# Optimization experiments

Hardware: AMD Instinct MI355X
Metric: run time of the kernel (lower is better)

The kernel has to match this reference:

```python
import jax, jax.numpy as jnp
import numpy as np

B, N, F, K = 512, 128, 128, 4


def setup_inputs() -> dict:
    key = jax.random.key(0)
    ks = jax.random.split(key, 12)
    # xavier-normal-ish scales
    s_rw = float(np.sqrt(2.0 / (F + F)))
    s_sw = float(np.sqrt(2.0 / (F + F)))
    inp = {
        "H": jax.random.normal(ks[0], (B, N, F), dtype=jnp.float32),
        "E": jax.random.uniform(ks[1], (B, N, N, K), dtype=jnp.float32),
        "RW1": jax.random.normal(ks[2], (F, F, K), dtype=jnp.float32) * s_rw,
        "SW1": jax.random.normal(ks[3], (F, F), dtype=jnp.float32) * s_sw,
        "RW2": jax.random.normal(ks[4], (F, F, K), dtype=jnp.float32) * s_rw,
        "SW2": jax.random.normal(ks[5], (F, F), dtype=jnp.float32) * s_sw,
        "RW3": jax.random.normal(ks[6], (F, F, K), dtype=jnp.float32) * s_rw,
        "SW3": jax.random.normal(ks[7], (F, F), dtype=jnp.float32) * s_sw,
        "W1": jax.random.normal(ks[8], (F, 20), dtype=jnp.float32) * float(np.sqrt(1.0 / F)),
        "b1": jnp.zeros((20,), dtype=jnp.float32),
        "W2": jax.random.normal(ks[9], (20, 1), dtype=jnp.float32) * float(np.sqrt(1.0 / 20)),
        "b2": jnp.zeros((1,), dtype=jnp.float32),
    }
    return inp


def _rgcn_conv(H, E, D, RW, SW):
    # einsum('bi,bijk,bjm,mnk->bin') done in two GEMM-shaped steps
    M = jnp.einsum('bijk,bjm->bimk', E, H)          # [B,N,F,K]
    msg = jnp.einsum('bimk,mnk->bin', M, RW)        # [B,N,F]
    return jax.nn.sigmoid(msg * D[:, :, None] + jnp.einsum('bij,jl->bil', H, SW))


def reference(H, E, RW1, SW1, RW2, SW2, RW3, SW3, W1, b1, W2, b2):
    # degree norm with self-loops: (E + eye)[b,i,:,:].sum() = E.sum((2,3)) + K
    k = jnp.asarray(E.shape[-1], dtype=E.dtype)
    D = 1.0 / (E.sum(axis=(2, 3)) + k)              # [B,N]
    H = _rgcn_conv(H, E, D, RW1, SW1)
    H = _rgcn_conv(H, E, D, RW2, SW2)
    H = _rgcn_conv(H, E, D, RW3, SW3)
    h = jnp.maximum(H @ W1 + b1, 0.1 * (H @ W1 + b1))  # LeakyReLU(0.1)
    score = jnp.mean(jax.nn.sigmoid(h @ W2 + b2))
    return score
```

## Files before the change

### kernel.cpp

```cpp
#include <hip/hip_runtime.h>
#include <math.h>

#define BB 512
#define NN 128
#define FF 128
#define KK 4

typedef __attribute__((ext_vector_type(8))) short bf16x8;
typedef __attribute__((ext_vector_type(4))) float f32x4;

__device__ inline unsigned short f2bf(float x) {
  union { float f; unsigned int u; } v; v.f = x;
  unsigned int r = v.u + 0x7fff + ((v.u >> 16) & 1);
  return (unsigned short)(r >> 16);
}
__device__ inline float bf2f(unsigned short h) {
  union { unsigned int u; float f; } v; v.u = ((unsigned int)h) << 16; return v.f;
}

__device__ inline void g2l16(const unsigned short* gptr, unsigned short* lptr) {
  __builtin_amdgcn_global_load_lds(
      (const __attribute__((address_space(1))) unsigned int*)gptr,
      (__attribute__((address_space(3))) unsigned int*)lptr, 16, 0, 0);
}

__global__ __launch_bounds__(256) void k_convE(const float* __restrict__ E,
                                               unsigned short* __restrict__ Eb,
                                               float* __restrict__ Dv) {
  int wave = threadIdx.x >> 6;
  int lane = threadIdx.x & 63;
  int row  = blockIdx.x * 4 + wave;
  const float* p = E + (size_t)row * 512 + lane * 8;
  f32x4 a = *(const f32x4*)p;
  f32x4 b = *(const f32x4*)(p + 4);
  float s = a[0] + a[1] + a[2] + a[3] + b[0] + b[1] + b[2] + b[3];
  #pragma unroll
  for (int off = 32; off > 0; off >>= 1) s += __shfl_down(s, off, 64);
  if (lane == 0) Dv[row] = 1.0f / (s + 4.0f);
  union { unsigned short h[8]; f32x4 v; } u;
  u.h[0] = f2bf(a[0]); u.h[1] = f2bf(a[1]); u.h[2] = f2bf(a[2]); u.h[3] = f2bf(a[3]);
  u.h[4] = f2bf(b[0]); u.h[5] = f2bf(b[1]); u.h[6] = f2bf(b[2]); u.h[7] = f2bf(b[3]);
  *(f32x4*)(Eb + (size_t)row * 512 + lane * 8) = u.v;
}

__global__ __launch_bounds__(256) void k_convH(const float* __restrict__ H,
                                               unsigned short* __restrict__ Hb) {
  size_t i = ((size_t)blockIdx.x * 256 + threadIdx.x) * 8;
  f32x4 a = *(const f32x4*)(H + i);
  f32x4 b = *(const f32x4*)(H + i + 4);
  union { unsigned short h[8]; f32x4 v; } u;
  u.h[0] = f2bf(a[0]); u.h[1] = f2bf(a[1]); u.h[2] = f2bf(a[2]); u.h[3] = f2bf(a[3]);
  u.h[4] = f2bf(b[0]); u.h[5] = f2bf(b[1]); u.h[6] = f2bf(b[2]); u.h[7] = f2bf(b[3]);
  *(f32x4*)(Hb + i) = u.v;
}

__global__ __launch_bounds__(256) void k_buildW(const float* __restrict__ RW,
                                                const float* __restrict__ SW,
                                                unsigned short* __restrict__ W2) {
  int idx = blockIdx.x * 256 + threadIdx.x;
  int m = idx & 127;
  int c = idx >> 7;
  float v = (c < 512) ? RW[m * 512 + c] : SW[m * 128 + (c - 512)];
  W2[idx] = f2bf(v);
}

#define GS_PITCH 132

__global__ __launch_bounds__(512, 2) void k_layer(
    const unsigned short* __restrict__ Eb,
    const unsigned short* __restrict__ Hin,
    const unsigned short* __restrict__ W2L,
    const float* __restrict__ Dv,
    unsigned short* __restrict__ Hout)
{
  __shared__ unsigned short Gs[128 * GS_PITCH];
  __shared__ unsigned short Es[128 * 128];

  const int b = blockIdx.x;
  const unsigned short* E_b = Eb  + (size_t)b * 65536;
  const unsigned short* H_b = Hin + (size_t)b * 16384;

  const int tid = threadIdx.x;
  const int w = tid >> 6, l = tid & 63;
  const int wr = w >> 1, wc = w & 1;
  const int lq = l >> 4, lm = l & 15;

  f32x4 macc[2][4] = {};

  for (int s = 0; s < 4; ++s) {
    if (s) __syncthreads();

    bf16x8 fa0[4], fb0[2];
    #pragma unroll
    for (int f = 0; f < 4; ++f)
      fa0[f] = *(const bf16x8*)(W2L + (w * 64 + f * 16 + lm) * 128 + lq * 8);
    #pragma unroll
    for (int g = 0; g < 2; ++g)
      fb0[g] = *(const bf16x8*)(H_b + (s * 32 + g * 16 + lm) * 128 + lq * 8);

    #pragma unroll
    for (int r = 0; r < 4; ++r) {
      int R   = r * 32 + w * 4 + (l >> 4);
      int cbg = (l & 15) ^ (R & 15);
      g2l16(E_b + R * 512 + s * 128 + cbg * 8,
            Es + (r * 32 + w * 4) * 128);
    }

    f32x4 gacc[4][2] = {};
    #pragma unroll
    for (int f = 0; f < 4; ++f)
      #pragma unroll
      for (int g = 0; g < 2; ++g)
        gacc[f][g] = __builtin_amdgcn_mfma_f32_16x16x32_bf16(fa0[f], fb0[g], gacc[f][g], 0, 0, 0);
    #pragma unroll
    for (int k0 = 32; k0 < 128; k0 += 32) {
      bf16x8 fa[4], fb[2];
      #pragma unroll
      for (int f = 0; f < 4; ++f)
        fa[f] = *(const bf16x8*)(W2L + (w * 64 + f * 16 + lm) * 128 + k0 + lq * 8);
      #pragma unroll
      for (int g = 0; g < 2; ++g)
        fb[g] = *(const bf16x8*)(H_b + (s * 32 + g * 16 + lm) * 128 + k0 + lq * 8);
      #pragma unroll
      for (int f = 0; f < 4; ++f)
        #pragma unroll
        for (int g = 0; g < 2; ++g)
          gacc[f][g] = __builtin_amdgcn_mfma_f32_16x16x32_bf16(fa[f], fb[g], gacc[f][g], 0, 0, 0);
    }
    #pragma unroll
    for (int f = 0; f < 4; ++f) {
      int n = w * 16 + f * 4 + lq;
      #pragma unroll
      for (int g = 0; g < 2; ++g) {
        int jl = g * 16 + lm;
        union { unsigned short h4[4]; uint2 v; } u;
        u.h4[0] = f2bf(gacc[f][g][0]); u.h4[1] = f2bf(gacc[f][g][1]);
        u.h4[2] = f2bf(gacc[f][g][2]); u.h4[3] = f2bf(gacc[f][g][3]);
        *(uint2*)(&Gs[n * GS_PITCH + jl * 4]) = u.v;
      }
    }
    __syncthreads();

    #pragma unroll
    for (int kt = 0; kt < 4; ++kt) {
      bf16x8 ea[2], fb[4];
      #pragma unroll
      for (int f = 0; f < 2; ++f) {
        int i  = wr * 32 + f * 16 + lm;
        int cb = (kt * 4 + lq) ^ lm;
        ea[f] = *(const bf16x8*)(Es + i * 128 + cb * 8);
      }
      #pragma unroll
      for (int g = 0; g < 4; ++g)
        fb[g] = *(const bf16x8*)(&Gs[(wc * 64 + g * 16 + lm) * GS_PITCH + kt * 32 + lq * 8]);
      #pragma unroll
      for (int f = 0; f < 2; ++f)
        #pragma unroll
        for (int g = 0; g < 4; ++g)
          macc[f][g] = __builtin_amdgcn_mfma_f32_16x16x32_bf16(ea[f], fb[g], macc[f][g], 0, 0, 0);
    }
  }

  f32x4 sacc[2][4] = {};
  #pragma unroll
  for (int k0 = 0; k0 < 128; k0 += 32) {
    bf16x8 fa[2], fb[4];
    #pragma unroll
    for (int f = 0; f < 2; ++f)
      fa[f] = *(const bf16x8*)(H_b + (wr * 32 + f * 16 + lm) * 128 + k0 + lq * 8);
    #pragma unroll
    for (int g = 0; g < 4; ++g)
      fb[g] = *(const bf16x8*)(W2L + (512 + wc * 64 + g * 16 + lm) * 128 + k0 + lq * 8);
    #pragma unroll
    for (int f = 0; f < 2; ++f)
      #pragma unroll
      for (int g = 0; g < 4; ++g)
        sacc[f][g] = __builtin_amdgcn_mfma_f32_16x16x32_bf16(fa[f], fb[g], sacc[f][g], 0, 0, 0);
  }

  const float* dvb = Dv + b * 128;
  __syncthreads();
  #pragma unroll
  for (int f = 0; f < 2; ++f) {
    int i0 = wr * 32 + f * 16 + lq * 4;
    f32x4 d = *(const f32x4*)(dvb + i0);
    #pragma unroll
    for (int g = 0; g < 4; ++g) {
      int n = wc * 64 + g * 16 + lm;
      #pragma unroll
      for (int r = 0; r < 4; ++r) {
        float v = fmaf(macc[f][g][r], d[r], sacc[f][g][r]);
        Es[(i0 + r) * 128 + n] = f2bf(1.0f / (1.0f + __expf(-v)));
      }
    }
  }
  __syncthreads();
  unsigned short* O_b = Hout + (size_t)b * 16384;
  {
    int off = tid * 32;
    f32x4 v0 = *(const f32x4*)(Es + off);
    f32x4 v1 = *(const f32x4*)(Es + off + 8);
    f32x4 v2 = *(const f32x4*)(Es + off + 16);
    f32x4 v3 = *(const f32x4*)(Es + off + 24);
    *(f32x4*)(O_b + off)      = v0;
    *(f32x4*)(O_b + off + 8)  = v1;
    *(f32x4*)(O_b + off + 16) = v2;
    *(f32x4*)(O_b + off + 24) = v3;
  }
}

__global__ __launch_bounds__(256) void k_mlp(
    const unsigned short* __restrict__ H,
    const float* __restrict__ W1,
    const float* __restrict__ b1,
    const float* __restrict__ W2,
    const float* __restrict__ b2,
    float* __restrict__ sumOut)
{
  __shared__ float W1s[128 * 20];
  __shared__ float b1s[20], W2s[20];
  __shared__ float red[256];
  for (int i = threadIdx.x; i < 2560; i += 256) W1s[i] = W1[i];
  if (threadIdx.x < 20) { b1s[threadIdx.x] = b1[threadIdx.x]; W2s[threadIdx.x] = W2[threadIdx.x]; }
  __syncthreads();

  int row = blockIdx.x * 256 + threadIdx.x;
  float h[20];
  #pragma unroll
  for (int j = 0; j < 20; ++j) h[j] = b1s[j];
  const unsigned short* hr = H + (size_t)row * 128;
  for (int m8 = 0; m8 < 128; m8 += 8) {
    f32x4 pk = *(const f32x4*)(hr + m8);
    const unsigned short* us = (const unsigned short*)&pk;
    #pragma unroll
    for (int e = 0; e < 8; ++e) {
      float x = bf2f(us[e]);
      #pragma unroll
      for (int j = 0; j < 20; ++j) h[j] = fmaf(x, W1s[(m8 + e) * 20 + j], h[j]);
    }
  }
  float v = b2[0];
  #pragma unroll
  for (int j = 0; j < 20; ++j) {
    float t = h[j];
    t = fmaxf(t, 0.1f * t);
    v = fmaf(t, W2s[j], v);
  }
  float s = 1.0f / (1.0f + __expf(-v));

  red[threadIdx.x] = s;
  __syncthreads();
  #pragma unroll
  for (int off = 128; off > 0; off >>= 1) {
    if (threadIdx.x < off) red[threadIdx.x] += red[threadIdx.x + off];
    __syncthreads();
  }
  if (threadIdx.x == 0) atomicAdd(sumOut, red[0]);
}

__global__ void k_final(const float* __restrict__ sum, float* __restrict__ out) {
  out[0] = sum[0] * (1.0f / 65536.0f);
}

extern "C" void kernel_launch(void* const* d_in, const int* in_sizes, int n_in,
                              void* d_out, int out_size, void* d_ws, size_t ws_size,
                              hipStream_t stream) {
  const float* H   = (const float*)d_in[0];
  const float* E   = (const float*)d_in[1];
  const float* RW1 = (const float*)d_in[2];
  const float* SW1 = (const float*)d_in[3];
  const float* RW2 = (const float*)d_in[4];
  const float* SW2 = (const float*)d_in[5];
  const float* RW3 = (const float*)d_in[6];
  const float* SW3 = (const float*)d_in[7];
  const float* W1  = (const float*)d_in[8];
  const float* b1  = (const float*)d_in[9];
  const float* W2  = (const float*)d_in[10];
  const float* b2  = (const float*)d_in[11];
  float* out = (float*)d_out;

  char* w = (char*)d_ws;
  float*          wsD   = (float*)w;           w += (size_t)65536 * 4;
  unsigned short* wsEb  = (unsigned short*)w;  w += (size_t)33554432 * 2;
  unsigned short* wsHa  = (unsigned short*)w;  w += (size_t)8388608 * 2;
  unsigned short* wsHb  = (unsigned short*)w;  w += (size_t)8388608 * 2;
  unsigned short* wsW2  = (unsigned short*)w;  w += (size_t)3 * 81920 * 2;
  float*          wsSum = (float*)w;           w += 256;

  k_convE<<<BB * NN / 4, 256, 0, stream>>>(E, wsEb, wsD);
  k_convH<<<8388608 / (256 * 8), 256, 0, stream>>>(H, wsHa);
  k_buildW<<<320, 256, 0, stream>>>(RW1, SW1, wsW2);
  k_buildW<<<320, 256, 0, stream>>>(RW2, SW2, wsW2 + 81920);
  k_buildW<<<320, 256, 0, stream>>>(RW3, SW3, wsW2 + 163840);
  hipMemsetAsync(wsSum, 0, sizeof(float), stream);

  k_layer<<<BB, 512, 0, stream>>>(wsEb, wsHa, wsW2,          wsD, wsHb);
  k_layer<<<BB, 512, 0, stream>>>(wsEb, wsHb, wsW2 + 81920,  wsD, wsHa);
  k_layer<<<BB, 512, 0, stream>>>(wsEb, wsHa, wsW2 + 163840, wsD, wsHb);

  k_mlp<<<BB * NN / 256, 256, 0, stream>>>(wsHb, W1, b1, W2, b2, wsSum);
  k_final<<<1, 1, 0, stream>>>(wsSum, out);
}
```

Before: 432.9 us.

## Fuse prep kernels and all three layers plus MLP into one megakernel

Merges the E/H conversion and weight-building kernels into a single prep launch. It also fuses the three RGCN layers, the MLP and the final reduction into one per-graph kernel that finishes with an atomic counter, removing launch gaps and the memset. Each graph's layers run back to back in the same block, so its E slice may stay hot in cache across layers. The cost is extra intermediate H buffers, a last-block-done pattern that relies on threadfence ordering, and MLP work that uses only 128 of the 512 threads.

```diff
diff --git a/kernel.cpp b/kernel.cpp
--- a/kernel.cpp
+++ b/kernel.cpp
@@ -5,6 +5,7 @@
 #define NN 128
 #define FF 128
 #define KK 4
+#define GS_PITCH 132
 
 typedef __attribute__((ext_vector_type(8))) short bf16x8;
 typedef __attribute__((ext_vector_type(4))) float f32x4;
@@ -24,63 +25,61 @@
       (__attribute__((address_space(3))) unsigned int*)lptr, 16, 0, 0);
 }
 
-__global__ __launch_bounds__(256) void k_convE(const float* __restrict__ E,
-                                               unsigned short* __restrict__ Eb,
-                                               float* __restrict__ Dv) {
-  int wave = threadIdx.x >> 6;
-  int lane = threadIdx.x & 63;
-  int row  = blockIdx.x * 4 + wave;
-  const float* p = E + (size_t)row * 512 + lane * 8;
-  f32x4 a = *(const f32x4*)p;
-  f32x4 b = *(const f32x4*)(p + 4);
-  float s = a[0] + a[1] + a[2] + a[3] + b[0] + b[1] + b[2] + b[3];
-  #pragma unroll
-  for (int off = 32; off > 0; off >>= 1) s += __shfl_down(s, off, 64);
-  if (lane == 0) Dv[row] = 1.0f / (s + 4.0f);
-  union { unsigned short h[8]; f32x4 v; } u;
-  u.h[0] = f2bf(a[0]); u.h[1] = f2bf(a[1]); u.h[2] = f2bf(a[2]); u.h[3] = f2bf(a[3]);
-  u.h[4] = f2bf(b[0]); u.h[5] = f2bf(b[1]); u.h[6] = f2bf(b[2]); u.h[7] = f2bf(b[3]);
-  *(f32x4*)(Eb + (size_t)row * 512 + lane * 8) = u.v;
-}
-
-__global__ __launch_bounds__(256) void k_convH(const float* __restrict__ H,
-                                               unsigned short* __restrict__ Hb) {
-  size_t i = ((size_t)blockIdx.x * 256 + threadIdx.x) * 8;
-  f32x4 a = *(const f32x4*)(H + i);
-  f32x4 b = *(const f32x4*)(H + i + 4);
-  union { unsigned short h[8]; f32x4 v; } u;
-  u.h[0] = f2bf(a[0]); u.h[1] = f2bf(a[1]); u.h[2] = f2bf(a[2]); u.h[3] = f2bf(a[3]);
-  u.h[4] = f2bf(b[0]); u.h[5] = f2bf(b[1]); u.h[6] = f2bf(b[2]); u.h[7] = f2bf(b[3]);
-  *(f32x4*)(Hb + i) = u.v;
-}
-
-__global__ __launch_bounds__(256) void k_buildW(const float* __restrict__ RW,
-                                                const float* __restrict__ SW,
-                                                unsigned short* __restrict__ W2) {
-  int idx = blockIdx.x * 256 + threadIdx.x;
-  int m = idx & 127;
-  int c = idx >> 7;
-  float v = (c < 512) ? RW[m * 512 + c] : SW[m * 128 + (c - 512)];
-  W2[idx] = f2bf(v);
-}
-
-#define GS_PITCH 132
-
-__global__ __launch_bounds__(512, 2) void k_layer(
-    const unsigned short* __restrict__ Eb,
-    const unsigned short* __restrict__ Hin,
-    const unsigned short* __restrict__ W2L,
-    const float* __restrict__ Dv,
-    unsigned short* __restrict__ Hout)
+__global__ __launch_bounds__(256) void k_prep(
+    const float* __restrict__ E, const float* __restrict__ H,
+    const float* __restrict__ RW1, const float* __restrict__ SW1,
+    const float* __restrict__ RW2, const float* __restrict__ SW2,
+    const float* __restrict__ RW3, const float* __restrict__ SW3,
+    unsigned short* __restrict__ Eb, unsigned short* __restrict__ Ha,
+    unsigned short* __restrict__ W2L, float* __restrict__ Dv,
+    float* __restrict__ Sum, int* __restrict__ Cnt)
 {
-  __shared__ unsigned short Gs[128 * GS_PITCH];
-  __shared__ unsigned short Es[128 * 128];
-
-  const int b = blockIdx.x;
-  const unsigned short* E_b = Eb  + (size_t)b * 65536;
-  const unsigned short* H_b = Hin + (size_t)b * 16384;
-
-  const int tid = threadIdx.x;
+  const int bid = blockIdx.x;
+  if (bid < 16384) {
+    int wave = threadIdx.x >> 6;
+    int lane = threadIdx.x & 63;
+    int row  = bid * 4 + wave;
+    const float* p = E + (size_t)row * 512 + lane * 8;
+    f32x4 a = *(const f32x4*)p;
+    f32x4 b = *(const f32x4*)(p + 4);
+    float s = a[0] + a[1] + a[2] + a[3] + b[0] + b[1] + b[2] + b[3];
+    #pragma unroll
+    for (int off = 32; off > 0; off >>= 1) s += __shfl_down(s, off, 64);
+    if (lane == 0) Dv[row] = 1.0f / (s + 4.0f);
+    union { unsigned short h[8]; f32x4 v; } u;
+    u.h[0] = f2bf(a[0]); u.h[1] = f2bf(a[1]); u.h[2] = f2bf(a[2]); u.h[3] = f2bf(a[3]);
+    u.h[4] = f2bf(b[0]); u.h[5] = f2bf(b[1]); u.h[6] = f2bf(b[2]); u.h[7] = f2bf(b[3]);
+    *(f32x4*)(Eb + (size_t)row * 512 + lane * 8) = u.v;
+  } else if (bid < 20480) {
+    size_t i = ((size_t)(bid - 16384) * 256 + threadIdx.x) * 8;
+    f32x4 a = *(const f32x4*)(H + i);
+    f32x4 b = *(const f32x4*)(H + i + 4);
+    union { unsigned short h[8]; f32x4 v; } u;
+    u.h[0] = f2bf(a[0]); u.h[1] = f2bf(a[1]); u.h[2] = f2bf(a[2]); u.h[3] = f2bf(a[3]);
+    u.h[4] = f2bf(b[0]); u.h[5] = f2bf(b[1]); u.h[6] = f2bf(b[2]); u.h[7] = f2bf(b[3]);
+    *(f32x4*)(Ha + i) = u.v;
+  } else {
+    int t2  = bid - 20480;
+    int tab = t2 / 320;
+    int idx = (t2 - tab * 320) * 256 + threadIdx.x;
+    int m = idx & 127;
+    int c = idx >> 7;
+    const float* RW = (tab == 0) ? RW1 : (tab == 1) ? RW2 : RW3;
+    const float* SW = (tab == 0) ? SW1 : (tab == 1) ? SW2 : SW3;
+    float v = (c < 512) ? RW[m * 512 + c] : SW[m * 128 + (c - 512)];
+    W2L[(size_t)tab * 81920 + idx] = f2bf(v);
+    if (t2 == 0 && threadIdx.x == 0) { *Sum = 0.0f; *Cnt = 0; }
+  }
+}
+
+__device__ __forceinline__ void layer_body(
+    const unsigned short* __restrict__ E_b,
+    const unsigned short* __restrict__ H_b,
+    const unsigned short* __restrict__ W2c,
+    const float* __restrict__ dvb,
+    unsigned short* __restrict__ O_b,
+    unsigned short* Gs, unsigned short* Es, const int tid)
+{
   const int w = tid >> 6, l = tid & 63;
   const int wr = w >> 1, wc = w & 1;
   const int lq = l >> 4, lm = l & 15;
@@ -93,7 +92,7 @@
     bf16x8 fa0[4], fb0[2];
     #pragma unroll
     for (int f = 0; f < 4; ++f)
-      fa0[f] = *(const bf16x8*)(W2L + (w * 64 + f * 16 + lm) * 128 + lq * 8);
+      fa0[f] = *(const bf16x8*)(W2c + (w * 64 + f * 16 + lm) * 128 + lq * 8);
     #pragma unroll
     for (int g = 0; g < 2; ++g)
       fb0[g] = *(const bf16x8*)(H_b + (s * 32 + g * 16 + lm) * 128 + lq * 8);
@@ -117,7 +116,7 @@
       bf16x8 fa[4], fb[2];
       #pragma unroll
       for (int f = 0; f < 4; ++f)
-        fa[f] = *(const bf16x8*)(W2L + (w * 64 + f * 16 + lm) * 128 + k0 + lq * 8);
+        fa[f] = *(const bf16x8*)(W2c + (w * 64 + f * 16 + lm) * 128 + k0 + lq * 8);
       #pragma unroll
       for (int g = 0; g < 2; ++g)
         fb[g] = *(const bf16x8*)(H_b + (s * 32 + g * 16 + lm) * 128 + k0 + lq * 8);
@@ -170,7 +169,7 @@
       fa[f] = *(const bf16x8*)(H_b + (wr * 32 + f * 16 + lm) * 128 + k0 + lq * 8);
     #pragma unroll
     for (int g = 0; g < 4; ++g)
-      fb[g] = *(const bf16x8*)(W2L + (512 + wc * 64 + g * 16 + lm) * 128 + k0 + lq * 8);
+      fb[g] = *(const bf16x8*)(W2c + (512 + wc * 64 + g * 16 + lm) * 128 + k0 + lq * 8);
     #pragma unroll
     for (int f = 0; f < 2; ++f)
       #pragma unroll
@@ -178,7 +177,6 @@
         sacc[f][g] = __builtin_amdgcn_mfma_f32_16x16x32_bf16(fa[f], fb[g], sacc[f][g], 0, 0, 0);
   }
 
-  const float* dvb = Dv + b * 128;
   __syncthreads();
   #pragma unroll
   for (int f = 0; f < 2; ++f) {
@@ -195,7 +193,6 @@
     }
   }
   __syncthreads();
-  unsigned short* O_b = Hout + (size_t)b * 16384;
   {
     int off = tid * 32;
     f32x4 v0 = *(const f32x4*)(Es + off);
@@ -207,64 +204,90 @@
     *(f32x4*)(O_b + off + 16) = v2;
     *(f32x4*)(O_b + off + 24) = v3;
   }
-}
-
-__global__ __launch_bounds__(256) void k_mlp(
-    const unsigned short* __restrict__ H,
-    const float* __restrict__ W1,
-    const float* __restrict__ b1,
-    const float* __restrict__ W2,
-    const float* __restrict__ b2,
-    float* __restrict__ sumOut)
+  __syncthreads();
+}
+
+__global__ __launch_bounds__(512, 2) void k_mega(
+    const unsigned short* __restrict__ Eb,
+    const unsigned short* __restrict__ Ha,
+    unsigned short* __restrict__ Hb,
+    unsigned short* __restrict__ Hc,
+    unsigned short* __restrict__ Hd,
+    const unsigned short* __restrict__ W2L,
+    const float* __restrict__ Dv,
+    const float* __restrict__ W1, const float* __restrict__ b1,
+    const float* __restrict__ W2w, const float* __restrict__ b2,
+    float* __restrict__ Sum, int* __restrict__ Cnt,
+    float* __restrict__ out)
 {
-  __shared__ float W1s[128 * 20];
-  __shared__ float b1s[20], W2s[20];
-  __shared__ float red[256];
-  for (int i = threadIdx.x; i < 2560; i += 256) W1s[i] = W1[i];
-  if (threadIdx.x < 20) { b1s[threadIdx.x] = b1[threadIdx.x]; W2s[threadIdx.x] = W2[threadIdx.x]; }
-  __syncthreads();
-
-  int row = blockIdx.x * 256 + threadIdx.x;
-  float h[20];
+  __shared__ unsigned short Gs[128 * GS_PITCH];
+  __shared__ unsigned short Es[128 * 128];
+
+  const int b = blockIdx.x;
+  const int tid = threadIdx.x;
+  const unsigned short* E_b = Eb + (size_t)b * 65536;
+  const float* dvb = Dv + b * 128;
+
+  layer_body(E_b, Ha + (size_t)b * 16384, W2L,          dvb, Hb + (size_t)b * 16384, Gs, Es, tid);
+  layer_body(E_b, Hb + (size_t)b * 16384, W2L + 81920,  dvb, Hc + (size_t)b * 16384, Gs, Es, tid);
+  layer_body(E_b, Hc + (size_t)b * 16384, W2L + 163840, dvb, Hd + (size_t)b * 16384, Gs, Es, tid);
+
+  float* W1s = (float*)Gs;
+  float* b1s = W1s + 2560;
+  float* W2s = b1s + 32;
+  float* red = W2s + 32;
+  for (int i = tid; i < 2560; i += 512) W1s[i] = W1[i];
+  if (tid < 20) { b1s[tid] = b1[tid]; W2s[tid] = W2w[tid]; }
+  __syncthreads();
+
+  float s = 0.0f;
+  if (tid < 128) {
+    const unsigned short* hr = Hd + (size_t)(b * 128 + tid) * 128;
+    float h[20];
+    #pragma unroll
+    for (int j = 0; j < 20; ++j) h[j] = b1s[j];
+    for (int m8 = 0; m8 < 128; m8 += 8) {
+      f32x4 pk = *(const f32x4*)(hr + m8);
+      const unsigned short* us = (const unsigned short*)&pk;
+      #pragma unroll
+      for (int e = 0; e < 8; ++e) {
+        float x = bf2f(us[e]);
+        #pragma unroll
+        for (int j = 0; j < 20; ++j) h[j] = fmaf(x, W1s[(m8 + e) * 20 + j], h[j]);
+      }
+    }
+    float v = b2[0];
+    #pragma unroll
+    for (int j = 0; j < 20; ++j) {
+      float t = h[j];
+      t = fmaxf(t, 0.1f * t);
+      v = fmaf(t, W2s[j], v);
+    }
+    s = 1.0f / (1.0f + __expf(-v));
+  }
+
+  red[tid] = s;
+  __syncthreads();
   #pragma unroll
-  for (int j = 0; j < 20; ++j) h[j] = b1s[j];
-  const unsigned short* hr = H + (size_t)row * 128;
-  for (int m8 = 0; m8 < 128; m8 += 8) {
-    f32x4 pk = *(const f32x4*)(hr + m8);
-    const unsigned short* us = (const unsigned short*)&pk;
-    #pragma unroll
-    for (int e = 0; e < 8; ++e) {
-      float x = bf2f(us[e]);
-      #pragma unroll
-      for (int j = 0; j < 20; ++j) h[j] = fmaf(x, W1s[(m8 + e) * 20 + j], h[j]);
-    }
-  }
-  float v = b2[0];
-  #pragma unroll
-  for (int j = 0; j < 20; ++j) {
-    float t = h[j];
-    t = fmaxf(t, 0.1f * t);
-    v = fmaf(t, W2s[j], v);
-  }
-  float s = 1.0f / (1.0f + __expf(-v));
-
-  red[threadIdx.x] = s;
-  __syncthreads();
-  #pragma unroll
-  for (int off = 128; off > 0; off >>= 1) {
-    if (threadIdx.x < off) red[threadIdx.x] += red[threadIdx.x + off];
+  for (int off = 256; off > 0; off >>= 1) {
+    if (tid < off) red[tid] += red[tid + off];
     __syncthreads();
   }
-  if (threadIdx.x == 0) atomicAdd(sumOut, red[0]);
-}
-
-__global__ void k_final(const float* __restrict__ sum, float* __restrict__ out) {
-  out[0] = sum[0] * (1.0f / 65536.0f);
+  if (tid == 0) {
+    atomicAdd(Sum, red[0]);
+    __threadfence();
+    int v = atomicAdd(Cnt, 1);
+    if (v == BB - 1) {
+      float tot = atomicAdd(Sum, 0.0f);
+      out[0] = tot * (1.0f / 65536.0f);
+    }
+  }
 }
 
 extern "C" void kernel_launch(void* const* d_in, const int* in_sizes, int n_in,
                               void* d_out, int out_size, void* d_ws, size_t ws_size,
                               hipStream_t stream) {
+  (void)in_sizes; (void)n_in; (void)out_size; (void)ws_size;
   const float* H   = (const float*)d_in[0];
   const float* E   = (const float*)d_in[1];
   const float* RW1 = (const float*)d_in[2];
@@ -284,20 +307,14 @@
   unsigned short* wsEb  = (unsigned short*)w;  w += (size_t)33554432 * 2;
   unsigned short* wsHa  = (unsigned short*)w;  w += (size_t)8388608 * 2;
   unsigned short* wsHb  = (unsigned short*)w;  w += (size_t)8388608 * 2;
+  unsigned short* wsHc  = (unsigned short*)w;  w += (size_t)8388608 * 2;
+  unsigned short* wsHd  = (unsigned short*)w;  w += (size_t)8388608 * 2;
   unsigned short* wsW2  = (unsigned short*)w;  w += (size_t)3 * 81920 * 2;
-  float*          wsSum = (float*)w;           w += 256;
-
-  k_convE<<<BB * NN / 4, 256, 0, stream>>>(E, wsEb, wsD);
-  k_convH<<<8388608 / (256 * 8), 256, 0, stream>>>(H, wsHa);
-  k_buildW<<<320, 256, 0, stream>>>(RW1, SW1, wsW2);
-  k_buildW<<<320, 256, 0, stream>>>(RW2, SW2, wsW2 + 81920);
-  k_buildW<<<320, 256, 0, stream>>>(RW3, SW3, wsW2 + 163840);
-  hipMemsetAsync(wsSum, 0, sizeof(float), stream);
-
-  k_layer<<<BB, 512, 0, stream>>>(wsEb, wsHa, wsW2,          wsD, wsHb);
-  k_layer<<<BB, 512, 0, stream>>>(wsEb, wsHb, wsW2 + 81920,  wsD, wsHa);
-  k_layer<<<BB, 512, 0, stream>>>(wsEb, wsHa, wsW2 + 163840, wsD, wsHb);
-
-  k_mlp<<<BB * NN / 256, 256, 0, stream>>>(wsHb, W1, b1, W2, b2, wsSum);
-  k_final<<<1, 1, 0, stream>>>(wsSum, out);
-}
+  float*          wsSum = (float*)w;           w += 64;
+  int*            wsCnt = (int*)w;             w += 64;
+
+  k_prep<<<21440, 256, 0, stream>>>(E, H, RW1, SW1, RW2, SW2, RW3, SW3,
+                                    wsEb, wsHa, wsW2, wsD, wsSum, wsCnt);
+  k_mega<<<BB, 512, 0, stream>>>(wsEb, wsHa, wsHb, wsHc, wsHd, wsW2, wsD,
+                                 W1, b1, W2, b2, wsSum, wsCnt, out);
+}
```

New measurement: 503.1 us. 16.2% more time.
